# Performance work log

Hardware: AMD Instinct MI355X
Metric: run time of the kernel (lower is better)

## Reference

```python
import jax, jax.numpy as jnp
import numpy as np

HEADS = 16
KERNEL_EPS = 1e-4  # performer_pytorch softmax_kernel eps
LN_EPS = 1e-5


def layernorm(x, g, b):
    m = jnp.mean(x, axis=-1, keepdims=True)
    v = jnp.var(x, axis=-1, keepdims=True)
    return (x - m) * jax.lax.rsqrt(v + LN_EPS) * g + b


def softmax_kernel(x, proj, is_query):
    # FAVOR+ positive random features (performer_pytorch softmax_kernel)
    d = x.shape[-1]
    m = proj.shape[0]
    xn = x * (d ** -0.25)                                   # data_normalizer * data
    dd = jnp.einsum('bhnd,md->bhnm', xn, proj)              # projected logits
    diag = 0.5 * jnp.sum(xn * xn, axis=-1, keepdims=True)   # ||x||^2/2 * normalizer^2
    if is_query:
        stab = jnp.max(dd, axis=-1, keepdims=True)
    else:
        stab = jnp.max(dd, axis=(-2, -1), keepdims=True)
    return (m ** -0.5) * (jnp.exp(dd - diag - stab) + KERNEL_EPS)


def favor_attention(x, proj, Wq, bq, Wk, bk, Wv, bv, Wo, bo):
    B, N, D = x.shape
    dh = D // HEADS

    def split(t):
        return t.reshape(B, N, HEADS, dh).transpose(0, 2, 1, 3)  # b h n d

    q = split(x @ Wq.T + bq)
    k = split(x @ Wk.T + bk)
    v = split(x @ Wv.T + bv)

    qp = softmax_kernel(q, proj, True)    # b h n m
    kp = softmax_kernel(k, proj, False)   # b h n m

    # non-causal linear attention: O(n*m*d)
    ksum = kp.sum(axis=2)                                    # b h m
    d_inv = 1.0 / jnp.einsum('bhnm,bhm->bhn', qp, ksum)      # b h n
    ctx = jnp.einsum('bhnm,bhnd->bhmd', kp, v)               # b h m d
    out = jnp.einsum('bhnm,bhmd,bhn->bhnd', qp, ctx, d_inv)  # b h n d

    out = out.transpose(0, 2, 1, 3).reshape(B, N, D)
    return out @ Wo.T + bo


def reference(x, proj, ln1_g, ln1_b, Wq, bq, Wk, bk, Wv, bv, Wo, bo,
              ln2_g, ln2_b, W1, b1, W2, b2):
    depth = proj.shape[0]
    for i in range(depth):
        h = layernorm(x, ln1_g[i], ln1_b[i])
        x = x + favor_attention(h, proj[i], Wq[i], bq[i], Wk[i], bk[i],
                                Wv[i], bv[i], Wo[i], bo[i])
        h = layernorm(x, ln2_g[i], ln2_b[i])
        x = x + (jax.nn.gelu(h @ W1[i].T + b1[i], approximate=False) @ W2[i].T + b2[i])
    return x


def _orthogonal_features(rng, m, d):
    # gaussian orthogonal random matrix, scaling=1 (rows scaled by sqrt(d))
    blocks = []
    for _ in range(m // d):
        qmat, _ = np.linalg.qr(rng.standard_normal((d, d)))
        blocks.append(qmat.T)
    return (np.sqrt(d) * np.concatenate(blocks, axis=0)).astype(np.float32)


def setup_inputs() -> dict:
    B, N, D, L, M, DH = 4, 2048, 1024, 4, 256, 64
    key = jax.random.key(0)
    ks = jax.random.split(key, 8)
    rng = np.random.default_rng(0)
    proj = jnp.asarray(np.stack([_orthogonal_features(rng, M, DH) for _ in range(L)]))
    s = 0.02
    return {
        'x': jax.random.normal(ks[0], (B, N, D), jnp.float32),
        'proj': proj,
        'ln1_g': jnp.ones((L, D), jnp.float32),
        'ln1_b': jnp.zeros((L, D), jnp.float32),
        'Wq': s * jax.random.normal(ks[1], (L, D, D), jnp.float32),
        'bq': jnp.zeros((L, D), jnp.float32),
        'Wk': s * jax.random.normal(ks[2], (L, D, D), jnp.float32),
        'bk': jnp.zeros((L, D), jnp.float32),
        'Wv': s * jax.random.normal(ks[3], (L, D, D), jnp.float32),
        'bv': jnp.zeros((L, D), jnp.float32),
        'Wo': s * jax.random.normal(ks[4], (L, D, D), jnp.float32),
        'bo': jnp.zeros((L, D), jnp.float32),
        'ln2_g': jnp.ones((L, D), jnp.float32),
        'ln2_b': jnp.zeros((L, D), jnp.float32),
        'W1': s * jax.random.normal(ks[5], (L, D, D), jnp.float32),
        'b1': jnp.zeros((L, D), jnp.float32),
        'W2': s * jax.random.normal(ks[6], (L, D, D), jnp.float32),
        'b2': jnp.zeros((L, D), jnp.float32),
    }
```

## Files before the change

kernel.cpp:

```cpp
#include <hip/hip_runtime.h>

#define B_    4
#define N_    2048
#define D_    1024
#define L_    4
#define M_    256
#define DH_   64
#define H_    16
#define BH_   64
#define ROWS_ 8192
#define WN_   1048576

typedef __bf16 bf16x8 __attribute__((ext_vector_type(8)));
typedef float  f32x4  __attribute__((ext_vector_type(4)));
typedef unsigned short u16;

__device__ __forceinline__ u16 f2b(float f){
  unsigned u = __float_as_uint(f);
  u += 0x7FFFu + ((u >> 16) & 1u);
  return (u16)(u >> 16);
}
__device__ __forceinline__ float b2f(u16 h){ return __uint_as_float(((unsigned)h) << 16); }

__device__ __forceinline__ void gload16(const u16* g, u16* l){
  __builtin_amdgcn_global_load_lds(
      (const __attribute__((address_space(1))) void*)g,
      (__attribute__((address_space(3))) void*)l, 16, 0, 0);
}

__global__ __launch_bounds__(256) void wcvt_k(const float* __restrict__ s, u16* __restrict__ d, long n){
  long i = ((long)blockIdx.x*256 + threadIdx.x)*4;
  if (i+3 < n){
    float4 v = *(const float4*)(s+i);
    d[i]=f2b(v.x); d[i+1]=f2b(v.y); d[i+2]=f2b(v.z); d[i+3]=f2b(v.w);
  } else {
    for(long j=i;j<n;j++) d[j]=f2b(s[j]);
  }
}

__global__ __launch_bounds__(256) void wcvt2_k(const float* __restrict__ s, u16* __restrict__ dbase, long n){
  long i = ((long)blockIdx.x*256 + threadIdx.x)*4;
  if (i < n){
    float4 v = *(const float4*)(s+i);
    long l = i >> 20, j = i & (WN_-1);
    u16* d = dbase + l*(6l*WN_) + j;
    d[0]=f2b(v.x); d[1]=f2b(v.y); d[2]=f2b(v.z); d[3]=f2b(v.w);
  }
}

__global__ void fillf_k(float* o, long n, float v){
  long i=(long)blockIdx.x*256+threadIdx.x; if(i<n) o[i]=v;
}

__global__ __launch_bounds__(256) void ln_k(const float* __restrict__ x,
    const float* __restrict__ g, const float* __restrict__ bt, u16* __restrict__ h){
  int row = blockIdx.x, t = threadIdx.x;
  const float* xr = x + (long)row*D_;
  float4 v = *(const float4*)(xr + t*4);
  float s  = v.x+v.y+v.z+v.w;
  float ss = v.x*v.x+v.y*v.y+v.z*v.z+v.w*v.w;
  #pragma unroll
  for (int m=1;m<64;m<<=1){ s += __shfl_xor(s,m); ss += __shfl_xor(ss,m); }
  __shared__ float ps[4][2];
  int w=t>>6;
  if ((t&63)==0){ ps[w][0]=s; ps[w][1]=ss; }
  __syncthreads();
  s  = ps[0][0]+ps[1][0]+ps[2][0]+ps[3][0];
  ss = ps[0][1]+ps[1][1]+ps[2][1]+ps[3][1];
  float mean = s*(1.0f/D_);
  float rs = rsqrtf(ss*(1.0f/D_) - mean*mean + 1e-5f);
  int c=t*4;
  u16* hr = h + (long)row*D_;
  hr[c+0]=f2b((v.x-mean)*rs*g[c+0]+bt[c+0]);
  hr[c+1]=f2b((v.y-mean)*rs*g[c+1]+bt[c+1]);
  hr[c+2]=f2b((v.z-mean)*rs*g[c+2]+bt[c+2]);
  hr[c+3]=f2b((v.w-mean)*rs*g[c+3]+bt[c+3]);
}

#define STAGE_PS(Ps, P) \
  _Pragma("unroll") \
  for (int i=0;i<8;i++){ \
    int c=threadIdx.x+i*256, row=c>>3, c8=c&7; \
    uint4 dv = *(const uint4*)((P) + row*64 + c8*8); \
    *(uint4*)((char*)(Ps) + (row<<7) + ((c8<<4)^((row&7)<<4))) = dv; \
  }
#define STAGE_XS_DG(Xs, X, b, hh, n0, dgL) \
  _Pragma("unroll") \
  for (int i=0;i<2;i++){ \
    int c=threadIdx.x+i*256, row=c>>3, c8=c&7; \
    uint4 dv = *(const uint4*)((X) + ((long)(b)*N_ + (n0)+row)*D_ + (hh)*DH_ + c8*8); \
    *(uint4*)((char*)(Xs) + (row<<7) + ((c8<<4)^((row&7)<<4))) = dv; \
    const u16* pe=(const u16*)&dv; \
    float sq=0.f; \
    _Pragma("unroll") \
    for (int e=0;e<8;e++){ float xv=b2f(pe[e]); sq += xv*xv; } \
    sq += __shfl_xor(sq,1); sq += __shfl_xor(sq,2); sq += __shfl_xor(sq,4); \
    if ((threadIdx.x&7)==0) (dgL)[row]=sq*0.0625f; \
  }
#define DD_MFMA(acc, Xs, Ps, w, lr, lg) \
  _Pragma("unroll") \
  for (int ks=0;ks<2;ks++){ \
    bf16x8 aF[4], bF[4]; \
    _Pragma("unroll") \
    for (int mi=0;mi<4;mi++){ \
      int row=mi*16+(lr); \
      aF[mi]=*(const bf16x8*)((const char*)(Xs) + (row<<7) + ((((ks<<2)+(lg))<<4)^((row&7)<<4))); \
    } \
    _Pragma("unroll") \
    for (int ni=0;ni<4;ni++){ \
      int row=(w)*64+ni*16+(lr); \
      bF[ni]=*(const bf16x8*)((const char*)(Ps) + (row<<7) + ((((ks<<2)+(lg))<<4)^((row&7)<<4))); \
    } \
    _Pragma("unroll") \
    for (int mi=0;mi<4;mi++) \
      _Pragma("unroll") \
      for (int ni=0;ni<4;ni++) \
        acc[mi][ni]=__builtin_amdgcn_mfma_f32_16x16x32_bf16(aF[mi],bF[ni],acc[mi][ni],0,0,0); \
  }

__global__ __launch_bounds__(256) void ddctx_k(
    const u16* __restrict__ Kb, const u16* __restrict__ P,
    const u16* __restrict__ Vb,
    float* __restrict__ part, float* __restrict__ kspart,
    float* __restrict__ msl, float* __restrict__ vsl, int zoff)
{
  __shared__ __align__(16) char smem[63760];
  u16* Ps = (u16*)smem;
  u16* Tr = (u16*)smem;
  u16* Xs = (u16*)(smem+36864);
  u16* Vs = (u16*)(smem+45056);
  u16* Tv = (u16*)(smem+54272);
  float* dgL = (float*)(smem+63488);
  float* rm  = (float*)(smem+63744);
  int t=threadIdx.x, w=t>>6, lane=t&63, lr=lane&15, lg=lane>>4;
  int zl=blockIdx.y, zg=zl+zoff, slot=blockIdx.x;
  int b=zg>>4, hh=zg&15;
  const float SN = 0.35355339059327373f;

  f32x4 cacc[4][4];
  #pragma unroll
  for (int mi=0;mi<4;mi++)
    #pragma unroll
    for (int ni=0;ni<4;ni++) cacc[mi][ni]=(f32x4){0.f,0.f,0.f,0.f};
  float ksp[4]={0.f,0.f,0.f,0.f};
  float vsacc=0.f;
  float mrun=-1e30f;

  for (int s=0;s<4;++s){
    int n0 = slot*256 + s*64;
    STAGE_PS(Ps, P); STAGE_XS_DG(Xs, Kb, b, hh, n0, dgL);
    {
      int row=t>>2, c16=(t&3)*16;
      const u16* src = Vb + ((long)b*N_ + n0+row)*D_ + hh*DH_ + c16;
      *(uint4*)&Tv[row*72+c16]   = *(const uint4*)src;
      *(uint4*)&Tv[row*72+c16+8] = *(const uint4*)(src+8);
    }
    __syncthreads();
    {
      int d=t>>2, nc=(t&3)*16;
      union { u16 u[16]; uint4 q[2]; } tv;
      #pragma unroll
      for (int j=0;j<16;j++) tv.u[j]=Tv[(nc+j)*72+d];
      *(uint4*)&Vs[d*72+nc]   = tv.q[0];
      *(uint4*)&Vs[d*72+nc+8] = tv.q[1];
    }
    f32x4 acc[4][4];
    #pragma unroll
    for (int mi=0;mi<4;mi++)
      #pragma unroll
      for (int ni=0;ni<4;ni++) acc[mi][ni]=(f32x4){0.f,0.f,0.f,0.f};
    DD_MFMA(acc, Xs, Ps, w, lr, lg);
    {
      float mx = acc[0][0][0];
      #pragma unroll
      for (int mi=0;mi<4;mi++)
        #pragma unroll
        for (int ni=0;ni<4;ni++)
          #pragma unroll
          for (int r=0;r<4;r++) mx=fmaxf(mx,acc[mi][ni][r]);
      #pragma unroll
      for (int m=1;m<64;m<<=1) mx = fmaxf(mx, __shfl_xor(mx,m));
      if (lane==0) rm[w]=mx;
    }
    __syncthreads();
    {
      int d=t>>2, q=t&3;
      float sv=0.f;
      #pragma unroll
      for (int j=0;j<16;j++) sv += b2f(Vs[d*72+q*16+j]);
      sv += __shfl_xor(sv,1); sv += __shfl_xor(sv,2);
      if (q==0) vsacc += sv;
    }
    {
      float tm = SN*fmaxf(fmaxf(rm[0],rm[1]),fmaxf(rm[2],rm[3]));
      float nm = fmaxf(mrun, tm);
      float sc = __expf(mrun - nm);
      mrun = nm;
      #pragma unroll
      for (int mi=0;mi<4;mi++)
        #pragma unroll
        for (int ni=0;ni<4;ni++)
          #pragma unroll
          for (int r=0;r<4;r++) cacc[mi][ni][r] *= sc;
      #pragma unroll
      for (int ni=0;ni<4;ni++) ksp[ni] *= sc;
    }
    #pragma unroll
    for (int mi=0;mi<4;mi++)
      #pragma unroll
      for (int ni=0;ni<4;ni++){
        int col = w*64+ni*16+lr;
        #pragma unroll
        for (int r=0;r<4;r++){
          int rw = mi*16+lg*4+r;
          float kp = 0.0625f*__expf(SN*acc[mi][ni][r] - dgL[rw] - mrun);
          Tr[col*72+rw] = f2b(kp);
          ksp[ni] += kp;
        }
      }
    __syncthreads();
    #pragma unroll
    for (int ks=0;ks<2;ks++){
      bf16x8 aF[4], bF[4];
      #pragma unroll
      for (int mi=0;mi<4;mi++)
        aF[mi]=*(const bf16x8*)(Tr + (w*64+mi*16+lr)*72 + ks*32 + lg*8);
      #pragma unroll
      for (int ni=0;ni<4;ni++)
        bF[ni]=*(const bf16x8*)(Vs + (ni*16+lr)*72 + ks*32 + lg*8);
      #pragma unroll
      for (int mi=0;mi<4;mi++)
        #pragma unroll
        for (int ni=0;ni<4;ni++)
          cacc[mi][ni]=__builtin_amdgcn_mfma_f32_16x16x32_bf16(aF[mi],bF[ni],cacc[mi][ni],0,0,0);
    }
    __syncthreads();
  }
  #pragma unroll
  for (int ni=0;ni<4;ni++){
    ksp[ni] += __shfl_xor(ksp[ni],16);
    ksp[ni] += __shfl_xor(ksp[ni],32);
  }
  long sb = (long)zl*8+slot;
  if (lane<16){
    float* kb_ = kspart + sb*256;
    #pragma unroll
    for (int ni=0;ni<4;ni++) kb_[w*64+ni*16+lane] = ksp[ni];
  }
  if (t==0) msl[sb]=mrun;
  if ((t&3)==0) vsl[sb*64 + (t>>2)] = vsacc;
  float* pb = part + sb*16384;
  #pragma unroll
  for (int mi=0;mi<4;mi++)
    #pragma unroll
    for (int ni=0;ni<4;ni++){
      int d = ni*16+lr;
      #pragma unroll
      for (int r=0;r<4;r++){
        int m = w*64+mi*16+lg*4+r;
        pb[m*64+d] = cacc[mi][ni][r];
      }
    }
}

__global__ __launch_bounds__(256) void ctxred2_k(
    const float* __restrict__ part, const float* __restrict__ kspart,
    const float* __restrict__ msl, const float* __restrict__ vsl,
    u16* __restrict__ ctxT, float* __restrict__ ksm)
{
  int z = blockIdx.x, t = threadIdx.x;
  const float* pz = part + (long)z*8*16384;
  const float* kz = kspart + (long)z*8*256;
  const float* mz = msl + (long)z*8;
  const float* vz = vsl + (long)z*8*64;
  float mg = mz[0];
  #pragma unroll
  for (int s8=1;s8<8;s8++) mg = fmaxf(mg, mz[s8]);
  float scl[8];
  #pragma unroll
  for (int s8=0;s8<8;s8++) scl[s8] = __expf(mz[s8]-mg);
  float s=0.f;
  #pragma unroll
  for (int s8=0;s8<8;s8++) s += kz[s8*256+t]*scl[s8];
  ksm[(long)z*256+t] = s + 0.0128f;
  __shared__ float vsT[64];
  if (t<64){
    float vv=0.f;
    #pragma unroll
    for (int s8=0;s8<8;s8++) vv += vz[s8*64+t];
    vsT[t]=vv;
  }
  __syncthreads();
  f32x4 r4[16];
  #pragma unroll
  for (int j=0;j<16;j++) r4[j]=(f32x4){0.f,0.f,0.f,0.f};
  #pragma unroll
  for (int s8=0;s8<8;s8++){
    const float* ps = pz + (long)s8*16384 + (long)t*64;
    float sc = scl[s8];
    #pragma unroll
    for (int j=0;j<16;j++){
      f32x4 v = *(const f32x4*)(ps + j*4);
      r4[j] += (f32x4){sc*v[0],sc*v[1],sc*v[2],sc*v[3]};
    }
  }
  u16 rb[64];
  #pragma unroll
  for (int j=0;j<16;j++){
    #pragma unroll
    for (int e=0;e<4;e++)
      rb[j*4+e]=f2b(r4[j][e] + 6.25e-6f*vsT[j*4+e]);
  }
  __shared__ __align__(16) u16 TT[64][72];
  u16* co = ctxT + (long)z*16384;
  for (int c=0;c<4;c++){
    __syncthreads();
    if ((t>>6)==c){
      int r=t&63;
      #pragma unroll
      for (int j=0;j<64;j+=8) *(uint4*)&TT[r][j] = *(const uint4*)&rb[j];
    }
    __syncthreads();
    int d=t>>2, mq=(t&3)*16;
    union { u16 u[16]; uint4 q[2]; } tmp;
    #pragma unroll
    for (int j=0;j<16;j++) tmp.u[j]=TT[mq+j][d];
    *(uint4*)(co + d*256 + c*64 + mq)     = tmp.q[0];
    *(uint4*)(co + d*256 + c*64 + mq + 8) = tmp.q[1];
  }
}

__global__ __launch_bounds__(256) void ddq_attn_k(
    const u16* __restrict__ Qb, const u16* __restrict__ P,
    const float* __restrict__ ksm, const u16* __restrict__ ctxT,
    u16* __restrict__ at, int zoff)
{
  __shared__ __align__(16) char smem[46336];
  u16*   Ps  = (u16*)smem;
  u16*   qpL = (u16*)smem;
  float* rdot= (float*)(smem+33792);
  float* dnvs= (float*)(smem+34816);
  u16*   Xs  = (u16*)(smem+36864);
  float* rm  = (float*)(smem+45056);
  float* dgL = (float*)(smem+46080);
  int t=threadIdx.x, w=t>>6, lane=t&63, lr=lane&15, lg=lane>>4;
  int zl=blockIdx.y, zg=zl+zoff, n0=blockIdx.x*64;
  int b=zg>>4, hh=zg&15;
  const float SN = 0.35355339059327373f;

  STAGE_PS(Ps, P); STAGE_XS_DG(Xs, Qb, b, hh, n0, dgL);
  __syncthreads();
  f32x4 acc[4][4];
  #pragma unroll
  for (int mi=0;mi<4;mi++)
    #pragma unroll
    for (int ni=0;ni<4;ni++) acc[mi][ni]=(f32x4){0.f,0.f,0.f,0.f};
  DD_MFMA(acc, Xs, Ps, w, lr, lg);
  float rmx[4][4];
  #pragma unroll
  for (int mi=0;mi<4;mi++)
    #pragma unroll
    for (int r=0;r<4;r++){
      float v = acc[mi][0][r];
      #pragma unroll
      for (int ni=1;ni<4;ni++) v=fmaxf(v, acc[mi][ni][r]);
      #pragma unroll
      for (int m=1;m<16;m<<=1) v = fmaxf(v, __shfl_xor(v,m));
      rmx[mi][r]=v;
    }
  if (lr==0){
    #pragma unroll
    for (int mi=0;mi<4;mi++)
      #pragma unroll
      for (int r=0;r<4;r++) rm[w*64 + mi*16 + lg*4 + r] = rmx[mi][r];
  }
  __syncthreads();
  const float* ksz = ksm + (long)zl*256;
  float kcol[4];
  #pragma unroll
  for (int ni=0;ni<4;ni++) kcol[ni] = ksz[w*64+ni*16+lr];
  float rd[4][4];
  #pragma unroll
  for (int mi=0;mi<4;mi++)
    #pragma unroll
    for (int r=0;r<4;r++){
      int rw = mi*16+lg*4+r;
      float st = fmaxf(fmaxf(rm[rw],rm[64+rw]),fmaxf(rm[128+rw],rm[192+rw]));
      float dgv = dgL[rw];
      float rsum = 0.f;
      #pragma unroll
      for (int ni=0;ni<4;ni++){
        int col = w*64+ni*16+lr;
        float qpv = 0.0625f*(__expf(SN*acc[mi][ni][r] - dgv - SN*st) + 1e-4f);
        qpL[rw*264+col] = f2b(qpv);
        rsum += qpv*kcol[ni];
      }
      rd[mi][r]=rsum;
    }
  #pragma unroll
  for (int mi=0;mi<4;mi++)
    #pragma unroll
    for (int r=0;r<4;r++){
      #pragma unroll
      for (int m=1;m<16;m<<=1) rd[mi][r] += __shfl_xor(rd[mi][r],m);
    }
  if (lr==0){
    #pragma unroll
    for (int mi=0;mi<4;mi++)
      #pragma unroll
      for (int r=0;r<4;r++) rdot[w*64 + mi*16+lg*4+r] = rd[mi][r];
  }
  __syncthreads();
  if (t<64) dnvs[t] = 1.0f/(rdot[t]+rdot[64+t]+rdot[128+t]+rdot[192+t]);
  __syncthreads();
  const u16* cz = ctxT + (long)zl*16384;
  f32x4 aacc[4];
  #pragma unroll
  for (int ni=0;ni<4;ni++) aacc[ni]=(f32x4){0.f,0.f,0.f,0.f};
  #pragma unroll
  for (int ks=0;ks<8;ks++){
    bf16x8 aF = *(const bf16x8*)(qpL + (w*16+lr)*264 + ks*32 + lg*8);
    #pragma unroll
    for (int ni=0;ni<4;ni++){
      bf16x8 bF = *(const bf16x8*)(cz + (ni*16+lr)*256 + ks*32 + lg*8);
      aacc[ni]=__builtin_amdgcn_mfma_f32_16x16x32_bf16(aF,bF,aacc[ni],0,0,0);
    }
  }
  #pragma unroll
  for (int ni=0;ni<4;ni++){
    #pragma unroll
    for (int r=0;r<4;r++){
      int n = n0 + w*16 + lg*4 + r;
      at[((long)b*N_ + n)*D_ + hh*64 + ni*16 + lr] = f2b(aacc[ni][r]*dnvs[w*16+lg*4+r]);
    }
  }
}

template<int EPI,bool XS>
__global__ __launch_bounds__(512,2) void gemm3_k(
    const u16* __restrict__ A, int lda,
    const u16* __restrict__ W, int ldw,
    const float* __restrict__ bias, const float* __restrict__ biasK, const float* __restrict__ biasV,
    void* __restrict__ Cv, int ldc, int K)
{
  constexpr int BM=256, BN=128;
  extern __shared__ __align__(16) u16 lds3[];
  u16* AsB = lds3;
  u16* BsB = lds3 + 3*BM*64;
  int t=threadIdx.x;
  int bx, by;
  if (XS){
    unsigned gx=gridDim.x, flat=blockIdx.y*gx+blockIdx.x;
    unsigned cpx=(gx*gridDim.y)>>3;
    unsigned s=(flat&7)*cpx + (flat>>3);
    bx = s % gx; by = s / gx;
  } else { bx = blockIdx.x; by = blockIdx.y; }
  const u16* Ab = A + (long)by*BM*lda;
  const u16* Wb = W + (long)bx*BN*ldw;
  int w=t>>6, lane=t&63, lr=lane&15, lg=lane>>4;
  int wr=w>>2, wc=w&3;
  int srow=lane>>3, swcol=((lane&7)^srow)*8;
  f32x4 acc[8][2];
  #pragma unroll
  for (int mi=0;mi<8;mi++)
    #pragma unroll
    for (int ni=0;ni<2;ni++) acc[mi][ni]=(f32x4){0.f,0.f,0.f,0.f};

  auto stage=[&](int kt, int sbuf){
    const u16* Ak = Ab + kt*64;
    u16* Ad = AsB + sbuf*(BM*64);
    #pragma unroll
    for (int i=0;i<4;i++){
      int rb=w*32+i*8;
      gload16(Ak + (long)(rb+srow)*lda + swcol, Ad + rb*64);
    }
    const u16* Bk = Wb + kt*64;
    u16* Bd = BsB + sbuf*(BN*64);
    #pragma unroll
    for (int i=0;i<2;i++){
      int rb=w*16+i*8;
      gload16(Bk + (long)(rb+srow)*ldw + swcol, Bd + rb*64);
    }
  };

  const int nK = K/64;
  stage(0,0); if (nK>1) stage(1,1);
  int rbuf=0, sbuf=2;
  for (int kt=0; kt<nK; ++kt){
    if (kt+1<nK) asm volatile("s_waitcnt vmcnt(6)" ::: "memory");
    else         asm volatile("s_waitcnt vmcnt(0)" ::: "memory");
    __builtin_amdgcn_s_barrier();
    if (kt+2<nK) stage(kt+2, sbuf);
    const u16* Al = AsB + rbuf*(BM*64);
    const u16* Bl = BsB + rbuf*(BN*64);
    bf16x8 aF[8][2], bF[2][2];
    #pragma unroll
    for (int ni=0;ni<2;ni++){
      int row=wc*32+ni*16+lr;
      #pragma unroll
      for (int ks=0;ks<2;ks++)
        bF[ni][ks]=*(const bf16x8*)((const char*)Bl + (row<<7) + ((((ks<<2)+lg)<<4)^((row&7)<<4)));
    }
    #pragma unroll
    for (int mi=0;mi<8;mi++){
      int row=wr*128+mi*16+lr;
      #pragma unroll
      for (int ks=0;ks<2;ks++)
        aF[mi][ks]=*(const bf16x8*)((const char*)Al + (row<<7) + ((((ks<<2)+lg)<<4)^((row&7)<<4)));
    }
    #pragma unroll
    for (int ks=0;ks<2;ks++)
      #pragma unroll
      for (int mi=0;mi<8;mi++)
        #pragma unroll
        for (int ni=0;ni<2;ni++)
          acc[mi][ni]=__builtin_amdgcn_mfma_f32_16x16x32_bf16(aF[mi][ks],bF[ni][ks],acc[mi][ni],0,0,0);
    rbuf = (rbuf==2)?0:rbuf+1;
    sbuf = (sbuf==2)?0:sbuf+1;
  }

  #pragma unroll
  for (int mi=0;mi<8;mi++){
    #pragma unroll
    for (int ni=0;ni<2;ni++){
      int col = bx*BN + wc*32 + ni*16 + lr;
      float bv = 0.0f;
      if (EPI==6){
        int seg = col>>10;
        const float* bp = (seg==0)?bias:((seg==1)?biasK:biasV);
        bv = bp[col&1023];
      } else {
        bv = bias[col];
      }
      #pragma unroll
      for (int r=0;r<4;r++){
        int row = by*BM + wr*128 + mi*16 + lg*4 + r;
        float v = acc[mi][ni][r];
        if (EPI==1){
          ((float*)Cv)[(long)row*ldc + col] += v+bv;
        } else if (EPI==2){
          float u=v+bv;
          ((u16*)Cv)[(long)row*ldc + col] = f2b(0.5f*u*(1.0f+erff(u*0.70710678118654752f)));
        } else {
          int seg = col>>10, c = col&1023;
          ((u16*)Cv)[(long)seg*((long)ROWS_*D_) + (long)row*D_ + c] = f2b(v+bv);
        }
      }
    }
  }
}

struct WS {
  u16 *wbuf, *pjb, *hb, *qb, *kb, *pbuf, *sh16, *ctxT;
  float *part, *kspart, *msl, *vsl, *ksm;
  size_t total;
};
static WS plan_ws(char* base, int allW, int CH){
  WS w; size_t off=0;
  auto al=[&](size_t b)->char*{ char* p=base+off; off=(off+b+255)&~(size_t)255; return p; };
  const size_t TB=(size_t)ROWS_*D_*2;
  w.wbuf=(u16*)al((allW?6ull*L_:6ull)*WN_*2);
  w.pjb =(u16*)al((size_t)L_*M_*DH_*2);
  w.hb  =(u16*)al(TB);
  w.qb  =(u16*)al(TB);
  w.kb  =(u16*)al(TB);
  w.pbuf=(u16*)al(TB);
  w.sh16=(u16*)al(TB);
  w.part=(float*)al((size_t)CH*8*M_*DH_*4);
  w.kspart=(float*)al((size_t)CH*8*M_*4);
  w.msl =(float*)al((size_t)CH*8*4);
  w.vsl =(float*)al((size_t)CH*8*DH_*4);
  w.ctxT=(u16*)al((size_t)BH_*DH_*M_*2);
  w.ksm =(float*)al((size_t)BH_*M_*4);
  w.total=off;
  return w;
}

extern "C" void kernel_launch(void* const* d_in, const int* in_sizes, int n_in,
                              void* d_out, int out_size, void* d_ws, size_t ws_size,
                              hipStream_t stream)
{
  const float* x    = (const float*)d_in[0];
  const float* proj = (const float*)d_in[1];
  const float* ln1g = (const float*)d_in[2];
  const float* ln1b = (const float*)d_in[3];
  const float* Wq   = (const float*)d_in[4];
  const float* bq   = (const float*)d_in[5];
  const float* Wk   = (const float*)d_in[6];
  const float* bk   = (const float*)d_in[7];
  const float* Wv   = (const float*)d_in[8];
  const float* bv   = (const float*)d_in[9];
  const float* Wo   = (const float*)d_in[10];
  const float* bo   = (const float*)d_in[11];
  const float* ln2g = (const float*)d_in[12];
  const float* ln2b = (const float*)d_in[13];
  const float* W1   = (const float*)d_in[14];
  const float* b1   = (const float*)d_in[15];
  const float* W2   = (const float*)d_in[16];
  const float* b2   = (const float*)d_in[17];

  char* base=(char*)d_ws;
  int allW=1, CH=64;
  WS w = plan_ws(base, 1, 64);
  if (w.total > ws_size){ CH=16; w = plan_ws(base, 1, 16); }
  if (w.total > ws_size){ allW=0; w = plan_ws(base, 0, 16); }
  if (w.total > ws_size){
    fillf_k<<<(out_size+255)/256,256,0,stream>>>((float*)d_out,(long)out_size,(float)(ws_size>>20));
    return;
  }
  const int NCH = BH_/CH;

  u16* vb = w.pbuf;
  u16* at = w.hb;
  u16* tm = w.sh16;

  wcvt_k<<<(L_*M_*DH_/4+255)/256,256,0,stream>>>(proj,w.pjb,(long)L_*M_*DH_);
  if (allW){
    const long na = (long)L_*WN_;
    const int g2 = (int)(na/4/256);
    wcvt2_k<<<g2,256,0,stream>>>(Wq, w.wbuf,         na);
    wcvt2_k<<<g2,256,0,stream>>>(Wk, w.wbuf+WN_,     na);
    wcvt2_k<<<g2,256,0,stream>>>(Wv, w.wbuf+2l*WN_,  na);
    wcvt2_k<<<g2,256,0,stream>>>(Wo, w.wbuf+3l*WN_,  na);
    wcvt2_k<<<g2,256,0,stream>>>(W1, w.wbuf+4l*WN_,  na);
    wcvt2_k<<<g2,256,0,stream>>>(W2, w.wbuf+5l*WN_,  na);
  }
  hipMemcpyAsync(d_out, x, (size_t)ROWS_*D_*4, hipMemcpyDeviceToDevice, stream);
  float* Xc = (float*)d_out;

  const long wn = (long)WN_;
  const int wg = (int)(wn/4/256);
  const size_t G3LDS = 3ull*(256+128)*64*2;
  dim3 gBig(D_/128, ROWS_/256, 1);
  dim3 gQKV(3*D_/128, ROWS_/256, 1);

  for (int l=0;l<L_;l++){
    u16* lw = w.wbuf + (allW ? (size_t)l*6*wn : 0);
    u16* wqkv=lw;  u16* wo=lw+3*wn;  u16* w1=lw+4*wn;  u16* w2=lw+5*wn;
    if (!allW){
      wcvt_k<<<wg,256,0,stream>>>(Wq+(size_t)l*wn,lw,wn);
      wcvt_k<<<wg,256,0,stream>>>(Wk+(size_t)l*wn,lw+wn,wn);
      wcvt_k<<<wg,256,0,stream>>>(Wv+(size_t)l*wn,lw+2*wn,wn);
      wcvt_k<<<wg,256,0,stream>>>(Wo+(size_t)l*wn,wo,wn);
      wcvt_k<<<wg,256,0,stream>>>(W1+(size_t)l*wn,w1,wn);
      wcvt_k<<<wg,256,0,stream>>>(W2+(size_t)l*wn,w2,wn);
    }
    const u16* pj = w.pjb + (size_t)l*M_*DH_;

    ln_k<<<ROWS_,256,0,stream>>>(Xc, ln1g+(size_t)l*D_, ln1b+(size_t)l*D_, w.hb);
    gemm3_k<6,true><<<gQKV,512,G3LDS,stream>>>(w.hb,D_, wqkv,D_,
        bq+(size_t)l*D_, bk+(size_t)l*D_, bv+(size_t)l*D_, w.qb,D_,D_);

    for (int ch=0; ch<NCH; ch++){
      int zoff = ch*CH;
      ddctx_k<<<dim3(8,CH),256,0,stream>>>(w.kb, pj, vb, w.part, w.kspart,
                                           w.msl, w.vsl, zoff);
      ctxred2_k<<<CH,256,0,stream>>>(w.part, w.kspart, w.msl, w.vsl,
                                     w.ctxT+(long)zoff*DH_*M_, w.ksm+(long)zoff*M_);
      ddq_attn_k<<<dim3(N_/64,CH),256,0,stream>>>(w.qb, pj,
                                                  w.ksm+(long)zoff*M_,
                                                  w.ctxT+(long)zoff*DH_*M_, at, zoff);
    }

    gemm3_k<1,true><<<gBig,512,G3LDS,stream>>>(at,D_, wo,D_,
        bo+(size_t)l*D_, nullptr, nullptr, Xc,D_,D_);
    ln_k<<<ROWS_,256,0,stream>>>(Xc, ln2g+(size_t)l*D_, ln2b+(size_t)l*D_, w.hb);
    gemm3_k<2,true><<<gBig,512,G3LDS,stream>>>(w.hb,D_, w1,D_,
        b1+(size_t)l*D_, nullptr, nullptr, tm,D_,D_);
    gemm3_k<1,true><<<gBig,512,G3LDS,stream>>>(tm,D_, w2,D_,
        b2+(size_t)l*D_, nullptr, nullptr, Xc,D_,D_);
  }
}
```

Baseline: 1.201 ms.

## Split ctx reduction across more blocks and reshape GEMM warp tiling

The context-reduction kernel now launches four blocks per head along the m dimension instead of one. Each thread sums a 16-wide slice of d, so the kernel gets more parallelism and far fewer registers per thread, and the multi-pass shared-memory transpose becomes a single pass. Separately, the GEMM warp layout changes from 2x4 warps with 128x32 sub-tiles to 4x2 warps with 64x64 sub-tiles. That squarer shape gives better fragment reuse: 8 LDS fragment loads per 16 MFMAs instead of 10.

```diff
diff --git a/kernel.cpp b/kernel.cpp
--- a/kernel.cpp
+++ b/kernel.cpp
@@ -268,7 +268,7 @@
     const float* __restrict__ msl, const float* __restrict__ vsl,
     u16* __restrict__ ctxT, float* __restrict__ ksm)
 {
-  int z = blockIdx.x, t = threadIdx.x;
+  int q = blockIdx.x, z = blockIdx.y, t = threadIdx.x;
   const float* pz = part + (long)z*8*16384;
   const float* kz = kspart + (long)z*8*256;
   const float* mz = msl + (long)z*8;
@@ -279,10 +279,6 @@
   float scl[8];
   #pragma unroll
   for (int s8=0;s8<8;s8++) scl[s8] = __expf(mz[s8]-mg);
-  float s=0.f;
-  #pragma unroll
-  for (int s8=0;s8<8;s8++) s += kz[s8*256+t]*scl[s8];
-  ksm[(long)z*256+t] = s + 0.0128f;
   __shared__ float vsT[64];
   if (t<64){
     float vv=0.f;
@@ -291,43 +287,43 @@
     vsT[t]=vv;
   }
   __syncthreads();
-  f32x4 r4[16];
-  #pragma unroll
-  for (int j=0;j<16;j++) r4[j]=(f32x4){0.f,0.f,0.f,0.f};
+  int ml = t&63, dg = t>>6;
+  int m  = q*64 + ml;
+  f32x4 r4[4];
+  #pragma unroll
+  for (int j=0;j<4;j++) r4[j]=(f32x4){0.f,0.f,0.f,0.f};
   #pragma unroll
   for (int s8=0;s8<8;s8++){
-    const float* ps = pz + (long)s8*16384 + (long)t*64;
+    const float* ps = pz + (long)s8*16384 + (long)m*64 + dg*16;
     float sc = scl[s8];
     #pragma unroll
-    for (int j=0;j<16;j++){
+    for (int j=0;j<4;j++){
       f32x4 v = *(const f32x4*)(ps + j*4);
       r4[j] += (f32x4){sc*v[0],sc*v[1],sc*v[2],sc*v[3]};
     }
   }
-  u16 rb[64];
-  #pragma unroll
-  for (int j=0;j<16;j++){
-    #pragma unroll
-    for (int e=0;e<4;e++)
-      rb[j*4+e]=f2b(r4[j][e] + 6.25e-6f*vsT[j*4+e]);
+  if (dg==0){
+    float s=0.f;
+    #pragma unroll
+    for (int s8=0;s8<8;s8++) s += kz[s8*256+m]*scl[s8];
+    ksm[(long)z*256+m] = s + 0.0128f;
   }
   __shared__ __align__(16) u16 TT[64][72];
-  u16* co = ctxT + (long)z*16384;
-  for (int c=0;c<4;c++){
-    __syncthreads();
-    if ((t>>6)==c){
-      int r=t&63;
-      #pragma unroll
-      for (int j=0;j<64;j+=8) *(uint4*)&TT[r][j] = *(const uint4*)&rb[j];
-    }
-    __syncthreads();
-    int d=t>>2, mq=(t&3)*16;
-    union { u16 u[16]; uint4 q[2]; } tmp;
-    #pragma unroll
-    for (int j=0;j<16;j++) tmp.u[j]=TT[mq+j][d];
-    *(uint4*)(co + d*256 + c*64 + mq)     = tmp.q[0];
-    *(uint4*)(co + d*256 + c*64 + mq + 8) = tmp.q[1];
-  }
+  #pragma unroll
+  for (int j=0;j<4;j++)
+    #pragma unroll
+    for (int e=0;e<4;e++){
+      int d = dg*16 + j*4 + e;
+      TT[d][ml] = f2b(r4[j][e] + 6.25e-6f*vsT[d]);
+    }
+  __syncthreads();
+  int d = t>>2, ms=(t&3)*16;
+  union { u16 u[16]; uint4 qq[2]; } tmp;
+  #pragma unroll
+  for (int j=0;j<16;j++) tmp.u[j]=TT[d][ms+j];
+  u16* co = ctxT + (long)z*16384 + d*256 + q*64 + ms;
+  *(uint4*)co     = tmp.qq[0];
+  *(uint4*)(co+8) = tmp.qq[1];
 }
 
 __global__ __launch_bounds__(256) void ddq_attn_k(
@@ -458,13 +454,13 @@
   const u16* Ab = A + (long)by*BM*lda;
   const u16* Wb = W + (long)bx*BN*ldw;
   int w=t>>6, lane=t&63, lr=lane&15, lg=lane>>4;
-  int wr=w>>2, wc=w&3;
+  int wr=w>>1, wc=w&1;
   int srow=lane>>3, swcol=((lane&7)^srow)*8;
-  f32x4 acc[8][2];
-  #pragma unroll
-  for (int mi=0;mi<8;mi++)
-    #pragma unroll
-    for (int ni=0;ni<2;ni++) acc[mi][ni]=(f32x4){0.f,0.f,0.f,0.f};
+  f32x4 acc[4][4];
+  #pragma unroll
+  for (int mi=0;mi<4;mi++)
+    #pragma unroll
+    for (int ni=0;ni<4;ni++) acc[mi][ni]=(f32x4){0.f,0.f,0.f,0.f};
 
   auto stage=[&](int kt, int sbuf){
     const u16* Ak = Ab + kt*64;
@@ -493,17 +489,17 @@
     if (kt+2<nK) stage(kt+2, sbuf);
     const u16* Al = AsB + rbuf*(BM*64);
     const u16* Bl = BsB + rbuf*(BN*64);
-    bf16x8 aF[8][2], bF[2][2];
-    #pragma unroll
-    for (int ni=0;ni<2;ni++){
-      int row=wc*32+ni*16+lr;
+    bf16x8 aF[4][2], bF[4][2];
+    #pragma unroll
+    for (int ni=0;ni<4;ni++){
+      int row=wc*64+ni*16+lr;
       #pragma unroll
       for (int ks=0;ks<2;ks++)
         bF[ni][ks]=*(const bf16x8*)((const char*)Bl + (row<<7) + ((((ks<<2)+lg)<<4)^((row&7)<<4)));
     }
     #pragma unroll
-    for (int mi=0;mi<8;mi++){
-      int row=wr*128+mi*16+lr;
+    for (int mi=0;mi<4;mi++){
+      int row=wr*64+mi*16+lr;
       #pragma unroll
       for (int ks=0;ks<2;ks++)
         aF[mi][ks]=*(const bf16x8*)((const char*)Al + (row<<7) + ((((ks<<2)+lg)<<4)^((row&7)<<4)));
@@ -511,19 +507,19 @@
     #pragma unroll
     for (int ks=0;ks<2;ks++)
       #pragma unroll
-      for (int mi=0;mi<8;mi++)
+      for (int mi=0;mi<4;mi++)
         #pragma unroll
-        for (int ni=0;ni<2;ni++)
+        for (int ni=0;ni<4;ni++)
           acc[mi][ni]=__builtin_amdgcn_mfma_f32_16x16x32_bf16(aF[mi][ks],bF[ni][ks],acc[mi][ni],0,0,0);
     rbuf = (rbuf==2)?0:rbuf+1;
     sbuf = (sbuf==2)?0:sbuf+1;
   }
 
   #pragma unroll
-  for (int mi=0;mi<8;mi++){
-    #pragma unroll
-    for (int ni=0;ni<2;ni++){
-      int col = bx*BN + wc*32 + ni*16 + lr;
+  for (int mi=0;mi<4;mi++){
+    #pragma unroll
+    for (int ni=0;ni<4;ni++){
+      int col = bx*BN + wc*64 + ni*16 + lr;
       float bv = 0.0f;
       if (EPI==6){
         int seg = col>>10;
@@ -534,7 +530,7 @@
       }
       #pragma unroll
       for (int r=0;r<4;r++){
-        int row = by*BM + wr*128 + mi*16 + lg*4 + r;
+        int row = by*BM + wr*64 + mi*16 + lg*4 + r;
         float v = acc[mi][ni][r];
         if (EPI==1){
           ((float*)Cv)[(long)row*ldc + col] += v+bv;
@@ -655,7 +651,7 @@
       int zoff = ch*CH;
       ddctx_k<<<dim3(8,CH),256,0,stream>>>(w.kb, pj, vb, w.part, w.kspart,
                                            w.msl, w.vsl, zoff);
-      ctxred2_k<<<CH,256,0,stream>>>(w.part, w.kspart, w.msl, w.vsl,
+      ctxred2_k<<<dim3(4,CH),256,0,stream>>>(w.part, w.kspart, w.msl, w.vsl,
                                      w.ctxT+(long)zoff*DH_*M_, w.ksm+(long)zoff*M_);
       ddq_attn_k<<<dim3(N_/64,CH),256,0,stream>>>(w.qb, pj,
                                                   w.ksm+(long)zoff*M_,
```

Measured after the change: 1.152 ms. -4.1%, faster.
